# Optimization experiments

Hardware: AMD Instinct MI355X
Metric: run time of the kernel (lower is better)

The kernel has to match this reference:

```python
import jax, jax.numpy as jnp
import numpy as np

B, C, H, W = 16, 512, 32, 32
NH, HD = 8, 64
CTX_DIM, L = 768, 512
EPS = 1e-5


def setup_inputs() -> dict:
    key = jax.random.key(0)
    ks = jax.random.split(key, 10)
    x = jax.random.normal(ks[0], (B, C, H, W), dtype=jnp.float32)
    context = jax.random.normal(ks[1], (B, L, CTX_DIM), dtype=jnp.float32)
    context_mask = jax.random.randint(ks[2], (B, L), 0, 2).astype(bool)
    context_mask = context_mask.at[:, 0].set(True)  # guarantee >=1 valid key per row
    s = 0.02
    ln_w = jnp.ones((C,), jnp.float32)
    ln_b = jnp.zeros((C,), jnp.float32)
    Wq = jax.random.normal(ks[3], (C, C), jnp.float32) * s
    Wk = jax.random.normal(ks[4], (C, C), jnp.float32) * s
    Wv = jax.random.normal(ks[5], (C, C), jnp.float32) * s
    Wo = jax.random.normal(ks[6], (C, C), jnp.float32) * s
    Wctx = jax.random.normal(ks[7], (C, CTX_DIM), jnp.float32) * s
    return {"x": x, "context": context, "context_mask": context_mask,
            "ln_w": ln_w, "ln_b": ln_b, "Wq": Wq, "Wk": Wk, "Wv": Wv,
            "Wo": Wo, "Wctx": Wctx}


def _layernorm(x, w, b):
    mu = jnp.mean(x, axis=-1, keepdims=True)
    var = jnp.mean(jnp.square(x - mu), axis=-1, keepdims=True)
    return (x - mu) * jax.lax.rsqrt(var + EPS) * w + b


def reference(x, context, context_mask, ln_w, ln_b, Wq, Wk, Wv, Wo, Wctx):
    b, c, h, w = x.shape
    n = h * w
    hidden = x.reshape(b, c, n).transpose(0, 2, 1)          # [b, n, c]
    hidden_norm = _layernorm(hidden, ln_w, ln_b)
    ctx = jnp.einsum('bld,cd->blc', context, Wctx)          # context_proj

    q = jnp.einsum('bnc,ec->bne', hidden_norm, Wq).reshape(b, n, NH, HD).transpose(0, 2, 1, 3)
    k = jnp.einsum('blc,ec->ble', ctx, Wk).reshape(b, -1, NH, HD).transpose(0, 2, 1, 3)
    v = jnp.einsum('blc,ec->ble', ctx, Wv).reshape(b, -1, NH, HD).transpose(0, 2, 1, 3)

    scale = HD ** -0.5
    scores = jnp.einsum('bhnd,bhld->bhnl', q, k) * scale    # [b,H,n,L]
    mask4 = context_mask[:, None, None, :]                  # [b,1,1,L]
    scores = jnp.where(mask4, scores, -jnp.inf)
    all_invalid = ~jnp.any(mask4, axis=-1, keepdims=True)   # [b,1,1,1]
    scores = jnp.where(all_invalid, 0.0, scores)
    attn = jax.nn.softmax(scores, axis=-1)
    attn = jnp.where(mask4, attn, 0.0)
    attn = jnp.where(all_invalid, 0.0, attn)

    out = jnp.einsum('bhnl,bhld->bhnd', attn, v)            # [b,H,n,hd]
    out = out.transpose(0, 2, 1, 3).reshape(b, n, c)
    out = jnp.einsum('bnc,ec->bne', out, Wo)
    out = out + hidden
    return out.transpose(0, 2, 1).reshape(b, c, h, w)
```

## Files before the change

kernel.cpp:

```cpp
#include <hip/hip_runtime.h>

#define B_   16
#define C_   512
#define N_   1024
#define L_   512
#define CTX_ 768
#define NH_  8
#define HD_  64
#define EPS_ 1e-5f

typedef short bfrag  __attribute__((ext_vector_type(8)));
typedef short bfrag4 __attribute__((ext_vector_type(4)));
typedef float f32x4  __attribute__((ext_vector_type(4)));

__device__ __forceinline__ ushort f2bf(float f) {
  union { float f; unsigned u; } v; v.f = f;
  unsigned r = v.u + 0x7fffu + ((v.u >> 16) & 1u);
  return (ushort)(r >> 16);
}

__device__ __forceinline__ f32x4 mfma16(bfrag a, bfrag b, f32x4 c) {
  return __builtin_amdgcn_mfma_f32_16x16x32_bf16(a, b, c, 0, 0, 0);
}
__device__ __forceinline__ f32x4 mfma16k16(bfrag4 a, bfrag4 b, f32x4 c) {
  return __builtin_amdgcn_mfma_f32_16x16x16bf16_1k(a, b, c, 0, 0, 0);
}
__device__ __forceinline__ unsigned cvt_pk_bf16(float lo, float hi) {
  unsigned d;
  asm("v_cvt_pk_bf16_f32 %0, %1, %2" : "=v"(d) : "v"(lo), "v"(hi));
  return d;
}

__device__ __forceinline__ void g2l16(const ushort* g, ushort* l) {
  __builtin_amdgcn_global_load_lds(
      (const __attribute__((address_space(1))) void*)g,
      (__attribute__((address_space(3))) void*)l, 16, 0, 0);
}

__global__ __launch_bounds__(256) void cast5_kernel(
    const float* __restrict__ s0, const float* __restrict__ s1,
    const float* __restrict__ s2, const float* __restrict__ s3,
    const float* __restrict__ s4,
    ushort* __restrict__ d0, ushort* __restrict__ d1, ushort* __restrict__ d2,
    ushort* __restrict__ d3, ushort* __restrict__ d4) {
  int i = blockIdx.x * 256 + threadIdx.x;
  const float* src; ushort* dst; int off;
  if      (i < 98304)  { src = s0; dst = d0; off = i; }
  else if (i < 163840) { src = s1; dst = d1; off = i - 98304; }
  else if (i < 229376) { src = s2; dst = d2; off = i - 163840; }
  else if (i < 294912) { src = s3; dst = d3; off = i - 229376; }
  else                 { src = s4; dst = d4; off = i - 294912; }
  float4 vv = ((const float4*)src)[off];
  ushort4 o;
  o.x = f2bf(vv.x); o.y = f2bf(vv.y); o.z = f2bf(vv.z); o.w = f2bf(vv.w);
  ((ushort4*)dst)[off] = o;
}

__global__ __launch_bounds__(1024) void ln_stats(const float* __restrict__ x,
                                                 float* __restrict__ mu_out,
                                                 float* __restrict__ rs_out) {
  const int b  = blockIdx.x;
  const int n0 = blockIdx.y * 64;
  const int tid = threadIdx.x;
  const int nx = tid & 63, cg = tid >> 6;
  const float* xb = x + (size_t)b * C_ * N_;

  float s = 0.f, s2 = 0.f;
  for (int c = cg; c < C_; c += 16) {
    float v = xb[(size_t)c * N_ + n0 + nx];
    s += v; s2 += v * v;
  }
  __shared__ float red[2][16][64];
  red[0][cg][nx] = s; red[1][cg][nx] = s2;
  __syncthreads();
  if (cg == 0) {
    float ss = 0.f, ss2 = 0.f;
#pragma unroll
    for (int i = 0; i < 16; ++i) { ss += red[0][i][nx]; ss2 += red[1][i][nx]; }
    float m  = ss * (1.f / C_);
    float var = ss2 * (1.f / C_) - m * m;
    mu_out[(size_t)b * N_ + n0 + nx] = m;
    rs_out[(size_t)b * N_ + n0 + nx] = rsqrtf(var + EPS_);
  }
}

__device__ __forceinline__ void gemm_core(const ushort* __restrict__ A,
                                          const ushort* __restrict__ W,
                                          int K, ushort* la, ushort* lb,
                                          f32x4 acc[4][4],
                                          int tid, int wm, int we, int col, int rg) {
  const int lane = tid & 63, w = tid >> 6;
  const int rloc = lane >> 2, pt = lane & 3;
  const int pts = pt ^ ((rloc >> 1) & 3);
  const int qsel = (rg ^ ((col >> 1) & 3)) * 8;

  for (int k0 = 0; k0 < K; k0 += 32) {
#pragma unroll
    for (int c = 0; c < 2; ++c) {
      const int chunk = w + c * 4;
      const int row = chunk * 16 + rloc;
      g2l16(A + (size_t)row * K + k0 + pts * 8, la + chunk * 512);
      g2l16(W + (size_t)row * K + k0 + pts * 8, lb + chunk * 512);
    }
    __syncthreads();
    bfrag af[4], bf[4];
#pragma unroll
    for (int i = 0; i < 4; ++i) {
      af[i] = *(const bfrag*)&la[(wm + i * 16 + col) * 32 + qsel];
      bf[i] = *(const bfrag*)&lb[(we + i * 16 + col) * 32 + qsel];
    }
#pragma unroll
    for (int i = 0; i < 4; ++i)
#pragma unroll
      for (int j = 0; j < 4; ++j)
        acc[i][j] = mfma16(af[i], bf[j], acc[i][j]);
    __syncthreads();
  }
}

__global__ __launch_bounds__(256) void gemm_kv(const ushort* __restrict__ A,
                                               const ushort* __restrict__ Wk,
                                               const ushort* __restrict__ Wv,
                                               ushort* __restrict__ Ko,
                                               ushort* __restrict__ Vo) {
  __shared__ ushort la[128 * 32];
  __shared__ ushort lb[128 * 32];
  const int isv = blockIdx.y >> 2;
  const ushort* W = isv ? Wv : Wk;
  ushort* out = isv ? Vo : Ko;
  const int m0 = blockIdx.x * 128, e0 = (blockIdx.y & 3) * 128;
  const int tid = threadIdx.x, lane = tid & 63, w = tid >> 6;
  const int wm = (w >> 1) * 64, we = (w & 1) * 64;
  const int col = lane & 15, rg = lane >> 4;

  f32x4 acc[4][4] = {};
  gemm_core(A + (size_t)m0 * C_, W + (size_t)e0 * C_, C_, la, lb, acc, tid, wm, we, col, rg);

#pragma unroll
  for (int i = 0; i < 4; ++i)
#pragma unroll
    for (int j = 0; j < 4; ++j)
#pragma unroll
      for (int r = 0; r < 4; ++r)
        out[(size_t)(m0 + wm + i * 16 + rg * 4 + r) * 512 + e0 + we + j * 16 + col] =
            f2bf(acc[i][j][r]);
}

__global__ __launch_bounds__(256) void gemm_res(const ushort* __restrict__ A,
                                                const ushort* __restrict__ W,
                                                const float* __restrict__ x,
                                                float* __restrict__ out) {
  __shared__ ushort la[128 * 32];
  __shared__ ushort lb[128 * 32];
  __shared__ float T[16][132];
  const int m0 = blockIdx.x * 128, e0 = blockIdx.y * 128;
  const int tid = threadIdx.x, lane = tid & 63, w = tid >> 6;
  const int wm = (w >> 1) * 64, we = (w & 1) * 64;
  const int col = lane & 15, rg = lane >> 4;

  f32x4 acc[4][4] = {};
  gemm_core(A + (size_t)m0 * C_, W + (size_t)e0 * C_, C_, la, lb, acc, tid, wm, we, col, rg);

  const int b = m0 >> 10, n0l = m0 & 1023;
#pragma unroll
  for (int g = 0; g < 8; ++g) {
    if ((w & 1) == (g >> 2)) {
      const int j = g & 3;
#pragma unroll
      for (int i = 0; i < 4; ++i)
        *(f32x4*)&T[col][wm + i * 16 + rg * 4] = acc[i][j];
    }
    __syncthreads();
    const int n = tid & 127;
    for (int cc = tid >> 7; cc < 16; cc += 2) {
      const int c = e0 + g * 16 + cc;
      const size_t idx = (size_t)b * C_ * N_ + (size_t)c * N_ + n0l + n;
      out[idx] = T[cc][n] + x[idx];
    }
    __syncthreads();
  }
}

__global__ __launch_bounds__(256) void gemm_ctx(const float* __restrict__ Ap,
                                                const ushort* __restrict__ W,
                                                ushort* __restrict__ outp) {
  __shared__ ushort la[128 * 40];
  __shared__ ushort lb[128 * 40];
  const int m0 = blockIdx.x * 128, e0 = blockIdx.y * 128;
  const int tid = threadIdx.x, lane = tid & 63, w = tid >> 6;
  const int wm = (w >> 1) * 64, we = (w & 1) * 64;
  const int col = lane & 15, rg = lane >> 4;
  const int srow = tid >> 1, sh = (tid & 1) * 16;
  const int K = CTX_;

  f32x4 acc[4][4] = {};

  for (int k0 = 0; k0 < K; k0 += 32) {
    {
      const float* ap = &Ap[(size_t)(m0 + srow) * K + k0 + sh];
      float4 f0 = ((const float4*)ap)[0];
      float4 f1 = ((const float4*)ap)[1];
      float4 f2 = ((const float4*)ap)[2];
      float4 f3 = ((const float4*)ap)[3];
      union { int4 v; ushort u[8]; } p0, p1;
      p0.u[0] = f2bf(f0.x); p0.u[1] = f2bf(f0.y); p0.u[2] = f2bf(f0.z); p0.u[3] = f2bf(f0.w);
      p0.u[4] = f2bf(f1.x); p0.u[5] = f2bf(f1.y); p0.u[6] = f2bf(f1.z); p0.u[7] = f2bf(f1.w);
      p1.u[0] = f2bf(f2.x); p1.u[1] = f2bf(f2.y); p1.u[2] = f2bf(f2.z); p1.u[3] = f2bf(f2.w);
      p1.u[4] = f2bf(f3.x); p1.u[5] = f2bf(f3.y); p1.u[6] = f2bf(f3.z); p1.u[7] = f2bf(f3.w);
      *(int4*)&la[srow * 40 + sh]     = p0.v;
      *(int4*)&la[srow * 40 + sh + 8] = p1.v;
      const ushort* wp = &W[(size_t)(e0 + srow) * K + k0 + sh];
      *(int4*)&lb[srow * 40 + sh]     = *(const int4*)wp;
      *(int4*)&lb[srow * 40 + sh + 8] = *(const int4*)(wp + 8);
    }
    __syncthreads();
    bfrag af[4], bf[4];
#pragma unroll
    for (int i = 0; i < 4; ++i) {
      af[i] = *(const bfrag*)&la[(wm + i * 16 + col) * 40 + rg * 8];
      bf[i] = *(const bfrag*)&lb[(we + i * 16 + col) * 40 + rg * 8];
    }
#pragma unroll
    for (int i = 0; i < 4; ++i)
#pragma unroll
      for (int j = 0; j < 4; ++j)
        acc[i][j] = mfma16(af[i], bf[j], acc[i][j]);
    __syncthreads();
  }

#pragma unroll
  for (int i = 0; i < 4; ++i)
#pragma unroll
    for (int j = 0; j < 4; ++j)
#pragma unroll
      for (int r = 0; r < 4; ++r)
        outp[(size_t)(m0 + wm + i * 16 + rg * 4 + r) * 512 + e0 + we + j * 16 + col] =
            f2bf(acc[i][j][r]);
}

__global__ __launch_bounds__(256) void gemm_lnq(const float* __restrict__ x,
                                                const float* __restrict__ mu,
                                                const float* __restrict__ rs,
                                                const float* __restrict__ lnw,
                                                const float* __restrict__ lnb,
                                                const ushort* __restrict__ W,
                                                ushort* __restrict__ out) {
  __shared__ ushort la[128 * 40];
  __shared__ ushort lb[128 * 40];
  const int m0 = blockIdx.x * 128, e0 = blockIdx.y * 128;
  const int b = m0 >> 10, n0l = m0 & 1023;
  const int tid = threadIdx.x, lane = tid & 63, w = tid >> 6;
  const int wm = (w >> 1) * 64, we = (w & 1) * 64;
  const int col = lane & 15, rg = lane >> 4;
  const int nloc = tid & 127, chalf = (tid >> 7) * 16;
  const int srow = tid >> 1, sh = (tid & 1) * 16;

  const float muv = mu[(size_t)b * N_ + n0l + nloc];
  const float rsv = rs[(size_t)b * N_ + n0l + nloc];
  const float nmr = -muv * rsv;
  const float* xb = x + (size_t)b * C_ * N_ + n0l + nloc;

  f32x4 acc[4][4] = {};

  for (int k0 = 0; k0 < C_; k0 += 32) {
    {
      union { int4 v[2]; ushort u[16]; } pk;
#pragma unroll
      for (int i = 0; i < 16; ++i) {
        const int c = k0 + chalf + i;
        const float xv = xb[(size_t)c * N_];
        const float t = fmaf(xv, rsv, nmr);
        pk.u[i] = f2bf(fmaf(t, lnw[c], lnb[c]));
      }
      *(int4*)&la[nloc * 40 + chalf]     = pk.v[0];
      *(int4*)&la[nloc * 40 + chalf + 8] = pk.v[1];
      const ushort* wp = &W[(size_t)(e0 + srow) * C_ + k0 + sh];
      *(int4*)&lb[srow * 40 + sh]     = *(const int4*)wp;
      *(int4*)&lb[srow * 40 + sh + 8] = *(const int4*)(wp + 8);
    }
    __syncthreads();
    bfrag af[4], bf[4];
#pragma unroll
    for (int i = 0; i < 4; ++i) {
      af[i] = *(const bfrag*)&la[(wm + i * 16 + col) * 40 + rg * 8];
      bf[i] = *(const bfrag*)&lb[(we + i * 16 + col) * 40 + rg * 8];
    }
#pragma unroll
    for (int i = 0; i < 4; ++i)
#pragma unroll
      for (int j = 0; j < 4; ++j)
        acc[i][j] = mfma16(af[i], bf[j], acc[i][j]);
    __syncthreads();
  }

#pragma unroll
  for (int i = 0; i < 4; ++i)
#pragma unroll
    for (int j = 0; j < 4; ++j)
#pragma unroll
      for (int r = 0; r < 4; ++r)
        out[(size_t)(m0 + wm + i * 16 + rg * 4 + r) * 512 + e0 + we + j * 16 + col] =
            f2bf(acc[i][j][r]);
}

__global__ __launch_bounds__(256) void attn_mfma(const ushort* __restrict__ q,
                                                 const ushort* __restrict__ k,
                                                 const ushort* __restrict__ v,
                                                 const int* __restrict__ mask,
                                                 ushort* __restrict__ o) {
  __shared__ ushort Kl[2][64 * 72];
  __shared__ ushort Vt[2][64 * 72];
  __shared__ float mlb[2][64];

  const int lin = blockIdx.x;
  const int hb = lin & 127, qb = lin >> 7;
  const int h = hb & 7, b = hb >> 3;
  const int q0 = qb * 128;
  const int tid = threadIdx.x, lane = tid & 63, w = tid >> 6;
  const int col = lane & 15, rg = lane >> 4;
  const int wq = w * 32;
  const float C1 = 0.18033688011112042f;

  bfrag qf[2][2];
#pragma unroll
  for (int mi = 0; mi < 2; ++mi)
#pragma unroll
    for (int kc = 0; kc < 2; ++kc)
      qf[mi][kc] = *(const bfrag*)
          &q[((size_t)b * N_ + q0 + wq + mi * 16 + col) * C_ + h * HD_ + kc * 32 + rg * 8];

  f32x4 oa[2][4] = {};
  float l_part[2] = {0.f, 0.f};

  {
#pragma unroll
    for (int it = 0; it < 2; ++it) {
      const int idx = it * 256 + tid;
      const int key = idx >> 3, part = idx & 7;
      *(int4*)&Kl[0][key * 72 + part * 8] =
          *(const int4*)&k[((size_t)b * L_ + key) * C_ + h * HD_ + part * 8];
    }
#pragma unroll
    for (int it = 0; it < 4; ++it) {
      const int idx = it * 256 + tid;
      const int key = idx & 63, d0 = (idx >> 6) * 4;
      ushort4 vv = *(const ushort4*)&v[((size_t)b * L_ + key) * C_ + h * HD_ + d0];
      Vt[0][(d0 + 0) * 72 + key] = vv.x;
      Vt[0][(d0 + 1) * 72 + key] = vv.y;
      Vt[0][(d0 + 2) * 72 + key] = vv.z;
      Vt[0][(d0 + 3) * 72 + key] = vv.w;
    }
    if (tid < 64) mlb[0][tid] = mask[b * L_ + tid] ? 0.f : -1e30f;
  }
  __syncthreads();

  for (int t = 0; t < 8; ++t) {
    const int cur = t & 1;
    int4 kreg[2];
    ushort4 vreg[4];
    float mreg = 0.f;
    if (t < 7) {
      const int l0n = (t + 1) * 64;
#pragma unroll
      for (int it = 0; it < 2; ++it) {
        const int idx = it * 256 + tid;
        const int key = idx >> 3, part = idx & 7;
        kreg[it] = *(const int4*)&k[((size_t)b * L_ + l0n + key) * C_ + h * HD_ + part * 8];
      }
#pragma unroll
      for (int it = 0; it < 4; ++it) {
        const int idx = it * 256 + tid;
        const int key = idx & 63, d0 = (idx >> 6) * 4;
        vreg[it] = *(const ushort4*)&v[((size_t)b * L_ + l0n + key) * C_ + h * HD_ + d0];
      }
      if (tid < 64) mreg = mask[b * L_ + l0n + tid] ? 0.f : -1e30f;
    }

    const ushort* Kc = &Kl[cur][0];
    const ushort* Vc = &Vt[cur][0];
    f32x4 s2[2][4] = {};
#pragma unroll
    for (int kc = 0; kc < 2; ++kc) {
      bfrag kf[4];
#pragma unroll
      for (int ni = 0; ni < 4; ++ni)
        kf[ni] = *(const bfrag*)&Kc[(ni * 16 + col) * 72 + kc * 32 + rg * 8];
#pragma unroll
      for (int mi = 0; mi < 2; ++mi)
#pragma unroll
        for (int ni = 0; ni < 4; ++ni)
          s2[mi][ni] = mfma16(kf[ni], qf[mi][kc], s2[mi][ni]);
    }
    bfrag4 pf[2][4];
#pragma unroll
    for (int ni = 0; ni < 4; ++ni) {
      const f32x4 bias4 = *(const f32x4*)&mlb[cur][ni * 16 + rg * 4];
#pragma unroll
      for (int mi = 0; mi < 2; ++mi) {
        const float p0 = exp2f(fmaf(s2[mi][ni][0], C1, bias4[0]));
        const float p1 = exp2f(fmaf(s2[mi][ni][1], C1, bias4[1]));
        const float p2 = exp2f(fmaf(s2[mi][ni][2], C1, bias4[2]));
        const float p3 = exp2f(fmaf(s2[mi][ni][3], C1, bias4[3]));
        l_part[mi] += (p0 + p1) + (p2 + p3);
        union { bfrag4 v; unsigned u[2]; } pk;
        pk.u[0] = cvt_pk_bf16(p0, p1);
        pk.u[1] = cvt_pk_bf16(p2, p3);
        pf[mi][ni] = pk.v;
      }
    }
#pragma unroll
    for (int ni = 0; ni < 4; ++ni) {
      bfrag4 vf[4];
#pragma unroll
      for (int di = 0; di < 4; ++di)
        vf[di] = *(const bfrag4*)&Vc[(di * 16 + col) * 72 + ni * 16 + rg * 4];
#pragma unroll
      for (int mi = 0; mi < 2; ++mi)
#pragma unroll
        for (int di = 0; di < 4; ++di)
          oa[mi][di] = mfma16k16(pf[mi][ni], vf[di], oa[mi][di]);
    }

    if (t < 7) {
      const int nb = cur ^ 1;
#pragma unroll
      for (int it = 0; it < 2; ++it) {
        const int idx = it * 256 + tid;
        const int key = idx >> 3, part = idx & 7;
        *(int4*)&Kl[nb][key * 72 + part * 8] = kreg[it];
      }
#pragma unroll
      for (int it = 0; it < 4; ++it) {
        const int idx = it * 256 + tid;
        const int key = idx & 63, d0 = (idx >> 6) * 4;
        Vt[nb][(d0 + 0) * 72 + key] = vreg[it].x;
        Vt[nb][(d0 + 1) * 72 + key] = vreg[it].y;
        Vt[nb][(d0 + 2) * 72 + key] = vreg[it].z;
        Vt[nb][(d0 + 3) * 72 + key] = vreg[it].w;
      }
      if (tid < 64) mlb[nb][tid] = mreg;
    }
    __syncthreads();
  }

  float linv[2][4];
#pragma unroll
  for (int mi = 0; mi < 2; ++mi) {
    float l = l_part[mi];
    l += __shfl_xor(l, 16);
    l += __shfl_xor(l, 32);
#pragma unroll
    for (int r = 0; r < 4; ++r) {
      int lv = __builtin_amdgcn_ds_bpermute((rg * 4 + r) * 4, __float_as_int(l));
      linv[mi][r] = 1.f / __int_as_float(lv);
    }
  }
#pragma unroll
  for (int mi = 0; mi < 2; ++mi)
#pragma unroll
    for (int r = 0; r < 4; ++r) {
      const size_t row = (size_t)b * N_ + q0 + wq + mi * 16 + rg * 4 + r;
#pragma unroll
      for (int di = 0; di < 4; ++di)
        o[row * C_ + h * HD_ + di * 16 + col] = f2bf(oa[mi][di][r] * linv[mi][r]);
    }
}

extern "C" void kernel_launch(void* const* d_in, const int* in_sizes, int n_in,
                              void* d_out, int out_size, void* d_ws, size_t ws_size,
                              hipStream_t stream) {
  (void)in_sizes; (void)n_in; (void)out_size; (void)ws_size;
  const float* x       = (const float*)d_in[0];
  const float* context = (const float*)d_in[1];
  const int*   mask    = (const int*)d_in[2];
  const float* ln_w    = (const float*)d_in[3];
  const float* ln_b    = (const float*)d_in[4];
  const float* Wq      = (const float*)d_in[5];
  const float* Wk      = (const float*)d_in[6];
  const float* Wv      = (const float*)d_in[7];
  const float* Wo      = (const float*)d_in[8];
  const float* Wctx    = (const float*)d_in[9];

  char* wsb = (char*)d_ws;
  ushort* qb    = (ushort*)(wsb + 0);
  ushort* kb    = (ushort*)(wsb + 16777216);
  ushort* vb    = (ushort*)(wsb + 25165824);
  ushort* atto  = (ushort*)(wsb + 33554432);
  ushort* ctx   = (ushort*)(wsb + 50331648);
  ushort* wctxb = (ushort*)(wsb + 58720256);
  ushort* wqb   = (ushort*)(wsb + 59506688);
  ushort* wkb   = (ushort*)(wsb + 60030976);
  ushort* wvb   = (ushort*)(wsb + 60555264);
  ushort* wob   = (ushort*)(wsb + 61079552);
  float*  mub   = (float*)(wsb + 61603840);
  float*  rsb   = (float*)(wsb + 61669376);

  cast5_kernel<<<1408, 256, 0, stream>>>(Wctx, Wq, Wk, Wv, Wo,
                                         wctxb, wqb, wkb, wvb, wob);
  ln_stats<<<dim3(B_, N_ / 64), 1024, 0, stream>>>(x, mub, rsb);
  gemm_ctx<<<dim3(64, 4), 256, 0, stream>>>(context, wctxb, ctx);
  gemm_kv<<<dim3(64, 8), 256, 0, stream>>>(ctx, wkb, wvb, kb, vb);
  gemm_lnq<<<dim3(128, 4), 256, 0, stream>>>(x, mub, rsb, ln_w, ln_b, wqb, qb);
  attn_mfma<<<1024, 256, 0, stream>>>(qb, kb, vb, mask, atto);
  gemm_res<<<dim3(128, 4), 256, 0, stream>>>(atto, wob, x, (float*)d_out);
}
```

Before: 163.8 us.

## Store V pre-transposed from the KV projection GEMM to simplify attention loads

New measurement: 158.5 us. -3.2%, faster.

```diff
diff --git a/kernel.cpp b/kernel.cpp
--- a/kernel.cpp
+++ b/kernel.cpp
@@ -122,12 +122,12 @@
                                                const ushort* __restrict__ Wk,
                                                const ushort* __restrict__ Wv,
                                                ushort* __restrict__ Ko,
-                                               ushort* __restrict__ Vo) {
+                                               ushort* __restrict__ Vt_g) {
   __shared__ ushort la[128 * 32];
   __shared__ ushort lb[128 * 32];
+  __shared__ float T[16][132];
   const int isv = blockIdx.y >> 2;
   const ushort* W = isv ? Wv : Wk;
-  ushort* out = isv ? Vo : Ko;
   const int m0 = blockIdx.x * 128, e0 = (blockIdx.y & 3) * 128;
   const int tid = threadIdx.x, lane = tid & 63, w = tid >> 6;
   const int wm = (w >> 1) * 64, we = (w & 1) * 64;
@@ -136,14 +136,34 @@
   f32x4 acc[4][4] = {};
   gemm_core(A + (size_t)m0 * C_, W + (size_t)e0 * C_, C_, la, lb, acc, tid, wm, we, col, rg);
 
-#pragma unroll
-  for (int i = 0; i < 4; ++i)
-#pragma unroll
-    for (int j = 0; j < 4; ++j)
-#pragma unroll
-      for (int r = 0; r < 4; ++r)
-        out[(size_t)(m0 + wm + i * 16 + rg * 4 + r) * 512 + e0 + we + j * 16 + col] =
-            f2bf(acc[i][j][r]);
+  if (!isv) {
+#pragma unroll
+    for (int i = 0; i < 4; ++i)
+#pragma unroll
+      for (int j = 0; j < 4; ++j)
+#pragma unroll
+        for (int r = 0; r < 4; ++r)
+          Ko[(size_t)(m0 + wm + i * 16 + rg * 4 + r) * 512 + e0 + we + j * 16 + col] =
+              f2bf(acc[i][j][r]);
+  } else {
+    const int b = m0 >> 9, l0 = m0 & 511;
+#pragma unroll
+    for (int g = 0; g < 8; ++g) {
+      if ((w & 1) == (g >> 2)) {
+        const int j = g & 3;
+#pragma unroll
+        for (int i = 0; i < 4; ++i)
+          *(f32x4*)&T[col][wm + i * 16 + rg * 4] = acc[i][j];
+      }
+      __syncthreads();
+      const int n = tid & 127;
+      for (int cc = tid >> 7; cc < 16; cc += 2) {
+        const int e = e0 + g * 16 + cc;
+        Vt_g[((size_t)b * 512 + e) * 512 + l0 + n] = f2bf(T[cc][n]);
+      }
+      __syncthreads();
+    }
+  }
 }
 
 __global__ __launch_bounds__(256) void gemm_res(const ushort* __restrict__ A,
@@ -305,7 +325,7 @@
 
 __global__ __launch_bounds__(256) void attn_mfma(const ushort* __restrict__ q,
                                                  const ushort* __restrict__ k,
-                                                 const ushort* __restrict__ v,
+                                                 const ushort* __restrict__ vt,
                                                  const int* __restrict__ mask,
                                                  ushort* __restrict__ o) {
   __shared__ ushort Kl[2][64 * 72];
@@ -341,14 +361,11 @@
           *(const int4*)&k[((size_t)b * L_ + key) * C_ + h * HD_ + part * 8];
     }
 #pragma unroll
-    for (int it = 0; it < 4; ++it) {
+    for (int it = 0; it < 2; ++it) {
       const int idx = it * 256 + tid;
-      const int key = idx & 63, d0 = (idx >> 6) * 4;
-      ushort4 vv = *(const ushort4*)&v[((size_t)b * L_ + key) * C_ + h * HD_ + d0];
-      Vt[0][(d0 + 0) * 72 + key] = vv.x;
-      Vt[0][(d0 + 1) * 72 + key] = vv.y;
-      Vt[0][(d0 + 2) * 72 + key] = vv.z;
-      Vt[0][(d0 + 3) * 72 + key] = vv.w;
+      const int d = idx >> 3, k8 = (idx & 7) * 8;
+      *(int4*)&Vt[0][d * 72 + k8] =
+          *(const int4*)&vt[((size_t)b * 512 + h * HD_ + d) * 512 + k8];
     }
     if (tid < 64) mlb[0][tid] = mask[b * L_ + tid] ? 0.f : -1e30f;
   }
@@ -357,7 +374,7 @@
   for (int t = 0; t < 8; ++t) {
     const int cur = t & 1;
     int4 kreg[2];
-    ushort4 vreg[4];
+    int4 vreg[2];
     float mreg = 0.f;
     if (t < 7) {
       const int l0n = (t + 1) * 64;
@@ -368,10 +385,10 @@
         kreg[it] = *(const int4*)&k[((size_t)b * L_ + l0n + key) * C_ + h * HD_ + part * 8];
       }
 #pragma unroll
-      for (int it = 0; it < 4; ++it) {
+      for (int it = 0; it < 2; ++it) {
         const int idx = it * 256 + tid;
-        const int key = idx & 63, d0 = (idx >> 6) * 4;
-        vreg[it] = *(const ushort4*)&v[((size_t)b * L_ + l0n + key) * C_ + h * HD_ + d0];
+        const int d = idx >> 3, k8 = (idx & 7) * 8;
+        vreg[it] = *(const int4*)&vt[((size_t)b * 512 + h * HD_ + d) * 512 + l0n + k8];
       }
       if (tid < 64) mreg = mask[b * L_ + l0n + tid] ? 0.f : -1e30f;
     }
@@ -430,13 +447,10 @@
         *(int4*)&Kl[nb][key * 72 + part * 8] = kreg[it];
       }
 #pragma unroll
-      for (int it = 0; it < 4; ++it) {
+      for (int it = 0; it < 2; ++it) {
         const int idx = it * 256 + tid;
-        const int key = idx & 63, d0 = (idx >> 6) * 4;
-        Vt[nb][(d0 + 0) * 72 + key] = vreg[it].x;
-        Vt[nb][(d0 + 1) * 72 + key] = vreg[it].y;
-        Vt[nb][(d0 + 2) * 72 + key] = vreg[it].z;
-        Vt[nb][(d0 + 3) * 72 + key] = vreg[it].w;
+        const int d = idx >> 3, k8 = (idx & 7) * 8;
+        *(int4*)&Vt[nb][d * 72 + k8] = vreg[it];
       }
       if (tid < 64) mlb[nb][tid] = mreg;
     }
```
